# Optimization experiments

Hardware: AMD Instinct MI355X
Metric: run time of the kernel (lower is better)

## Reference

```python
import jax, jax.numpy as jnp
import numpy as np

B, T, CTX, D, L, H, FF, NMODES = 1024, 512, 23, 320, 5, 8, 1280, 48
DH = D // H
EPS = 1e-5


def layernorm(x, w, b):
    m = jnp.mean(x, axis=-1, keepdims=True)
    v = jnp.mean(jnp.square(x - m), axis=-1, keepdims=True)
    return (x - m) * jax.lax.rsqrt(v + EPS) * w + b


def cheb_sum(x, c):
    """sum_n c[:, n] * T_n(x) via the Chebyshev recurrence, fused with the
    reduction (Clenshaw-style accumulation, no (B,T,N+1) intermediate).
    x: (B,T) in [-1,1], c: (B, N+1)."""
    t_prev = jnp.ones_like(x)           # T_0
    t_cur = x                           # T_1
    acc = c[:, 0:1] * t_prev + c[:, 1:2] * t_cur

    def step(carry, cn):
        tp, tc, a = carry
        tn = 2.0 * x * tc - tp          # T_{n+1}
        return (tc, tn, a + cn[:, None] * tn), None

    (_, _, acc), _ = jax.lax.scan(step, (t_prev, t_cur, acc),
                                  jnp.swapaxes(c[:, 2:], 0, 1))
    return acc


def _forward(k_norm, ctx, W_e, b_e, cls, ln1_w, ln1_b, W_in, b_in, W_out, b_out,
             ln2_w, ln2_b, W1, b1, W2, b2, hln_w, hln_b, Wh1, bh1, Wh2, bh2):
    Bc = ctx.shape[0]
    # elem_proj: Linear(1, D) applied per scalar token -> (B, CTX, D)
    tok = ctx[..., None] * W_e + b_e
    x = jnp.concatenate([jnp.broadcast_to(cls, (Bc, 1, D)), tok], axis=1)  # (B, 24, D)

    def layer(x, p):
        l1w, l1b, win, bin_, wout, bout, l2w, l2b, w1, b1_, w2, b2_ = p
        # --- pre-norm self attention ---
        h = layernorm(x, l1w, l1b)
        qkv = h @ win.T + bin_                      # (B, S, 3D)
        q, k, v = jnp.split(qkv, 3, axis=-1)
        S = x.shape[1]
        q = q.reshape(Bc, S, H, DH)
        k = k.reshape(Bc, S, H, DH)
        v = v.reshape(Bc, S, H, DH)
        scores = jnp.einsum('bqhd,bkhd->bhqk', q, k) / np.sqrt(DH).astype(np.float32)
        a = jax.nn.softmax(scores, axis=-1)
        o = jnp.einsum('bhqk,bkhd->bqhd', a, v).reshape(Bc, S, D)
        x = x + o @ wout.T + bout
        # --- pre-norm FFN ---
        h2 = layernorm(x, l2w, l2b)
        x = x + jax.nn.gelu(h2 @ w1.T + b1_, approximate=False) @ w2.T + b2_
        return x, None

    x, _ = jax.lax.scan(layer, x, (ln1_w, ln1_b, W_in, b_in, W_out, b_out,
                                   ln2_w, ln2_b, W1, b1, W2, b2))
    h = layernorm(x[:, 0], hln_w, hln_b)            # CLS pooling + head LN
    c = jax.nn.gelu(h @ Wh1.T + bh1, approximate=False) @ Wh2.T + bh2  # (B, N+1)
    z = cheb_sum(k_norm, c)
    return jax.nn.sigmoid(z)


def setup_inputs() -> dict:
    key = jax.random.key(0)
    ks = jax.random.split(key, 24)
    rn = lambda k, sh, s=0.02: jax.random.normal(k, sh, jnp.float32) * s
    return {
        'k_norm': jax.random.uniform(ks[0], (B, T), jnp.float32, -1.0, 1.0),
        'ctx': jax.random.normal(ks[1], (B, CTX), jnp.float32),
        'W_e': rn(ks[2], (D,), 0.5),
        'b_e': jnp.zeros((D,), jnp.float32),
        'cls': rn(ks[3], (1, 1, D)),
        'ln1_w': jnp.ones((L, D), jnp.float32),
        'ln1_b': jnp.zeros((L, D), jnp.float32),
        'W_in': rn(ks[4], (L, 3 * D, D)),
        'b_in': jnp.zeros((L, 3 * D), jnp.float32),
        'W_out': rn(ks[5], (L, D, D)),
        'b_out': jnp.zeros((L, D), jnp.float32),
        'ln2_w': jnp.ones((L, D), jnp.float32),
        'ln2_b': jnp.zeros((L, D), jnp.float32),
        'W1': rn(ks[6], (L, FF, D)),
        'b1': jnp.zeros((L, FF), jnp.float32),
        'W2': rn(ks[7], (L, D, FF)),
        'b2': jnp.zeros((L, D), jnp.float32),
        'hln_w': jnp.ones((D,), jnp.float32),
        'hln_b': jnp.zeros((D,), jnp.float32),
        'Wh1': rn(ks[8], (D, D)),
        'bh1': jnp.zeros((D,), jnp.float32),
        'Wh2': rn(ks[9], (NMODES + 1, D)),
        'bh2': jnp.zeros((NMODES + 1,), jnp.float32),
    }


def reference(k_norm, ctx, W_e, b_e, cls, ln1_w, ln1_b, W_in, b_in, W_out, b_out,
              ln2_w, ln2_b, W1, b1, W2, b2, hln_w, hln_b, Wh1, bh1, Wh2, bh2):
    return _forward(k_norm, ctx, W_e, b_e, cls, ln1_w, ln1_b, W_in, b_in, W_out,
                    b_out, ln2_w, ln2_b, W1, b1, W2, b2, hln_w, hln_b, Wh1, bh1,
                    Wh2, bh2)
```

## Files before the change

kernel.cpp:

```cpp
#include <hip/hip_runtime.h>
#include <hip/hip_bf16.h>
#include <math.h>

#define B_SZ 1024
#define T_SZ 512
#define CTX_N 23
#define D 320
#define L_LAYERS 5
#define H 8
#define FF 1280
#define NM1 49
#define S 24
#define DH 40
#define M_ROWS (B_SZ * S)

typedef unsigned short ushort_t;
typedef __attribute__((ext_vector_type(8))) short bfrag8;
typedef __attribute__((ext_vector_type(4))) float facc4;

__device__ __forceinline__ float wave_sum(float v) {
#pragma unroll
  for (int off = 32; off > 0; off >>= 1) v += __shfl_xor(v, off, 64);
  return v;
}

__device__ __forceinline__ float gelu_fast(float x) {
  float t = __builtin_amdgcn_exp2f(x * (2.30211416f + 0.10294404f * x * x));
  return x - x * __builtin_amdgcn_rcpf(t + 1.0f);
}

__device__ __forceinline__ ushort_t f2b(float x) {
  __hip_bfloat16 h = __float2bfloat16(x);
  return *reinterpret_cast<ushort_t*>(&h);
}

__device__ __forceinline__ float b2f(ushort_t u) {
  __hip_bfloat16 h = *reinterpret_cast<__hip_bfloat16*>(&u);
  return __bfloat162float(h);
}

#define GLOAD_LDS16(g, l)                                     \
  __builtin_amdgcn_global_load_lds(                           \
      (const __attribute__((address_space(1))) void*)(g),     \
      (__attribute__((address_space(3))) void*)(l), 16, 0, 0)

__global__ __launch_bounds__(256) void conv_all(
    const float* __restrict__ w_in, const float* __restrict__ w_out,
    const float* __restrict__ w1, const float* __restrict__ w2,
    const float* __restrict__ wh1, ushort_t* __restrict__ dst) {
  int i = blockIdx.x * 256 + threadIdx.x;
  const float* src;
  int off;
  if (i < 384000)       { src = w_in;  off = i; }
  else if (i < 512000)  { src = w_out; off = i - 384000; }
  else if (i < 1024000) { src = w1;    off = i - 512000; }
  else if (i < 1536000) { src = w2;    off = i - 1024000; }
  else                  { src = wh1;   off = i - 1536000; }
  float4 v = ((const float4*)src)[off];
  ushort4 o;
  o.x = f2b(v.x); o.y = f2b(v.y); o.z = f2b(v.z); o.w = f2b(v.w);
  ((ushort4*)dst)[i] = o;
}

__global__ __launch_bounds__(256) void embed_kernel(
    const float* __restrict__ ctx, const float* __restrict__ W_e,
    const float* __restrict__ b_e, const float* __restrict__ cls,
    float* __restrict__ x) {
  int idx = blockIdx.x * 256 + threadIdx.x;
  int d = idx % D;
  int s = (idx / D) % S;
  int b = idx / (D * S);
  float v;
  if (s == 0)
    v = cls[d];
  else
    v = ctx[b * CTX_N + (s - 1)] * W_e[d] + b_e[d];
  x[idx] = v;
}

__global__ __launch_bounds__(256) void ln_kernel(
    const float* __restrict__ X, const float* __restrict__ w,
    const float* __restrict__ b, ushort_t* __restrict__ Y,
    int inStride, int outStride) {
  int wv = threadIdx.x >> 6;
  int lane = threadIdx.x & 63;
  int row = blockIdx.x * 4 + wv;
  const float* xr = X + (size_t)row * inStride;
  float v[5];
#pragma unroll
  for (int i = 0; i < 5; i++) v[i] = xr[lane + 64 * i];
  float s = v[0] + v[1] + v[2] + v[3] + v[4];
  s = wave_sum(s);
  float m = s * (1.0f / (float)D);
  float sq = 0.f;
#pragma unroll
  for (int i = 0; i < 5; i++) { float d0 = v[i] - m; sq += d0 * d0; }
  sq = wave_sum(sq);
  float inv = 1.0f / sqrtf(sq * (1.0f / (float)D) + 1e-5f);
  ushort_t* yr = Y + (size_t)row * outStride;
#pragma unroll
  for (int i = 0; i < 5; i++) {
    int d = lane + 64 * i;
    yr[d] = f2b((v[i] - m) * inv * w[d] + b[d]);
  }
}

template <int EPI, int NT, int MT>
__global__ __launch_bounds__(256, 3) void gemm_mfma(
    const ushort_t* __restrict__ A, const ushort_t* __restrict__ W,
    const float* __restrict__ bias, const float* __restrict__ R,
    float* __restrict__ C, ushort_t* __restrict__ Cb, int M, int N, int K) {
  constexpr int BM_ = MT * 32, BK = 64;
  constexpr int BN = 32 * NT;
  constexpr int AR = BM_ / 32;
  constexpr int WR = BN / 32;
  __shared__ __align__(16) ushort_t As[BM_ * BK];
  __shared__ __align__(16) ushort_t Ws[BN * BK];

  int tid = threadIdx.x;
  int lane = tid & 63;
  int wv = tid >> 6;
  int wvM = wv & 1, wvN = wv >> 1;
  int laneM = lane & 15;
  int kgrp = lane >> 4;
  int sA = laneM & 7;

  int nbx = gridDim.x;
  int lid = blockIdx.x + nbx * blockIdx.y;
  int nchunk = nbx >> 3;
  int mb = (lid & 7) * nchunk + ((lid >> 3) % nchunk);
  int nb = (lid >> 3) / nchunk;
  int m0 = mb * BM_;
  int n0 = nb * BN;

  facc4 acc[MT][NT];
#pragma unroll
  for (int mt = 0; mt < MT; mt++)
#pragma unroll
    for (int nt = 0; nt < NT; nt++) acc[mt][nt] = (facc4){0.f, 0.f, 0.f, 0.f};

  int srow = tid >> 3;
  int jg = (tid & 7) ^ (srow & 7);
  const ushort_t* Ag = A + (size_t)(m0 + srow) * K + jg * 8;
  const ushort_t* Wg = W + (size_t)(n0 + srow) * K + jg * 8;

  for (int k0 = 0; k0 < K; k0 += BK) {
#pragma unroll
    for (int r = 0; r < AR; r++)
      GLOAD_LDS16(Ag + (size_t)r * 32 * K + k0, As + r * 2048 + tid * 8);
#pragma unroll
    for (int r = 0; r < WR; r++)
      GLOAD_LDS16(Wg + (size_t)r * 32 * K + k0, Ws + r * 2048 + tid * 8);
    __syncthreads();
#pragma unroll
    for (int kc = 0; kc < 2; kc++) {
      int jcol = ((kc * 4 + kgrp) ^ sA) * 8;
      bfrag8 af[MT];
#pragma unroll
      for (int mt = 0; mt < MT; mt++) {
        int row = wvM * (MT * 16) + mt * 16 + laneM;
        af[mt] = *(const bfrag8*)&As[row * 64 + jcol];
      }
#pragma unroll
      for (int nt = 0; nt < NT; nt++) {
        int nrow = wvN * (BN / 2) + nt * 16 + laneM;
        bfrag8 bf = *(const bfrag8*)&Ws[nrow * 64 + jcol];
#pragma unroll
        for (int mt = 0; mt < MT; mt++)
          acc[mt][nt] = __builtin_amdgcn_mfma_f32_16x16x32_bf16(
              bf, af[mt], acc[mt][nt], 0, 0, 0);
      }
    }
    __syncthreads();
  }

#pragma unroll
  for (int mt = 0; mt < MT; mt++) {
    int m = m0 + wvM * (MT * 16) + mt * 16 + laneM;
#pragma unroll
    for (int nt = 0; nt < NT; nt++) {
      int n = n0 + wvN * (BN / 2) + nt * 16 + kgrp * 4;
      float4 bv = *(const float4*)(bias + n);
      facc4 a = acc[mt][nt];
      float v0 = a[0] + bv.x, v1 = a[1] + bv.y, v2 = a[2] + bv.z,
            v3 = a[3] + bv.w;
      size_t off = (size_t)m * N + n;
      if constexpr (EPI == 1) {
        ushort4 o;
        o.x = f2b(gelu_fast(v0)); o.y = f2b(gelu_fast(v1));
        o.z = f2b(gelu_fast(v2)); o.w = f2b(gelu_fast(v3));
        *(ushort4*)(Cb + off) = o;
      } else if constexpr (EPI == 2) {
        float4 r = *(const float4*)(R + off);
        float4 o = {v0 + r.x, v1 + r.y, v2 + r.z, v3 + r.w};
        *(float4*)(C + off) = o;
      } else if constexpr (EPI == 3) {
        float4 o = {gelu_fast(v0), gelu_fast(v1), gelu_fast(v2),
                    gelu_fast(v3)};
        *(float4*)(C + off) = o;
      } else {
        ushort4 o;
        o.x = f2b(v0); o.y = f2b(v1); o.z = f2b(v2); o.w = f2b(v3);
        *(ushort4*)(Cb + off) = o;
      }
    }
  }
}

__global__ __launch_bounds__(256) void attn_kernel(
    const ushort_t* __restrict__ qkv, ushort_t* __restrict__ o) {
  int b = blockIdx.x >> 3;
  int h = blockIdx.x & 7;
  __shared__ __align__(16) float q[S][44];
  __shared__ __align__(16) float v[S][44];
  __shared__ __align__(16) float kT[DH][28];
  __shared__ __align__(16) float sc[S][28];
  int tid = threadIdx.x;
  const ushort_t* base = qkv + (size_t)b * S * (3 * D) + h * DH;

  for (int idx = tid; idx < 720; idx += 256) {
    int t = idx / 240;
    int r = idx % 240;
    int s = r / 10, dg = r % 10;
    ushort4 u = *(const ushort4*)(base + (size_t)s * (3 * D) + t * D + dg * 4);
    float4 f = {b2f(u.x), b2f(u.y), b2f(u.z), b2f(u.w)};
    if (t == 0) {
      *(float4*)&q[s][dg * 4] = f;
    } else if (t == 2) {
      *(float4*)&v[s][dg * 4] = f;
    } else {
      kT[dg * 4 + 0][s] = f.x;
      kT[dg * 4 + 1][s] = f.y;
      kT[dg * 4 + 2][s] = f.z;
      kT[dg * 4 + 3][s] = f.w;
    }
  }
  __syncthreads();

  if (tid < 144) {
    int i = tid / 6, jg = tid % 6;
    facc4 acc = {0.f, 0.f, 0.f, 0.f};
#pragma unroll
    for (int d = 0; d < DH; d++) {
      float qv = q[i][d];
      float4 kv = *(const float4*)&kT[d][jg * 4];
      acc[0] += qv * kv.x; acc[1] += qv * kv.y;
      acc[2] += qv * kv.z; acc[3] += qv * kv.w;
    }
    const float sca = 0.15811388300841897f;
    float4 ov = {acc[0] * sca, acc[1] * sca, acc[2] * sca, acc[3] * sca};
    *(float4*)&sc[i][jg * 4] = ov;
  }
  __syncthreads();

  if (tid < S) {
    float mx = -1e30f;
#pragma unroll
    for (int j = 0; j < S; j++) mx = fmaxf(mx, sc[tid][j]);
    float sum = 0.f;
#pragma unroll
    for (int j = 0; j < S; j++) {
      float e = __expf(sc[tid][j] - mx);
      sc[tid][j] = e;
      sum += e;
    }
    float rr = 1.0f / sum;
#pragma unroll
    for (int j = 0; j < S; j++) sc[tid][j] *= rr;
  }
  __syncthreads();

  if (tid < 240) {
    int i = tid / 10, dg = tid % 10;
    facc4 acc = {0.f, 0.f, 0.f, 0.f};
#pragma unroll
    for (int j = 0; j < S; j++) {
      float p = sc[i][j];
      float4 vv = *(const float4*)&v[j][dg * 4];
      acc[0] += p * vv.x; acc[1] += p * vv.y;
      acc[2] += p * vv.z; acc[3] += p * vv.w;
    }
    ushort4 ov;
    ov.x = f2b(acc[0]); ov.y = f2b(acc[1]);
    ov.z = f2b(acc[2]); ov.w = f2b(acc[3]);
    *(ushort4*)(o + (size_t)b * S * D + (size_t)i * D + h * DH + dg * 4) = ov;
  }
}

__global__ __launch_bounds__(256) void head_cheb(
    const float* __restrict__ g, const float* __restrict__ Wh2,
    const float* __restrict__ bh2, const float* __restrict__ k_norm,
    float* __restrict__ out) {
  int b = blockIdx.x;
  __shared__ float gs[D];
  __shared__ float cs[NM1];
  int tid = threadIdx.x;
  for (int i = tid; i < D; i += 256) gs[i] = g[(size_t)b * D + i];
  __syncthreads();
  if (tid < NM1) {
    const float* wr = Wh2 + (size_t)tid * D;
    float s = bh2[tid];
    for (int d = 0; d < D; d++) s += gs[d] * wr[d];
    cs[tid] = s;
  }
  __syncthreads();
  for (int t = tid; t < T_SZ; t += 256) {
    float xv = k_norm[(size_t)b * T_SZ + t];
    float tp = 1.f, tc = xv;
    float acc = cs[0] + cs[1] * xv;
#pragma unroll
    for (int n = 2; n < NM1; n++) {
      float tn = 2.f * xv * tc - tp;
      acc += cs[n] * tn;
      tp = tc;
      tc = tn;
    }
    out[(size_t)b * T_SZ + t] = 1.f / (1.f + expf(-acc));
  }
}

extern "C" void kernel_launch(void* const* d_in, const int* in_sizes, int n_in,
                              void* d_out, int out_size, void* d_ws,
                              size_t ws_size, hipStream_t stream) {
  const float* k_norm = (const float*)d_in[0];
  const float* ctx    = (const float*)d_in[1];
  const float* W_e    = (const float*)d_in[2];
  const float* b_e    = (const float*)d_in[3];
  const float* cls    = (const float*)d_in[4];
  const float* ln1_w  = (const float*)d_in[5];
  const float* ln1_b  = (const float*)d_in[6];
  const float* W_in   = (const float*)d_in[7];
  const float* b_in   = (const float*)d_in[8];
  const float* W_out  = (const float*)d_in[9];
  const float* b_out  = (const float*)d_in[10];
  const float* ln2_w  = (const float*)d_in[11];
  const float* ln2_b  = (const float*)d_in[12];
  const float* W1     = (const float*)d_in[13];
  const float* b1     = (const float*)d_in[14];
  const float* W2     = (const float*)d_in[15];
  const float* b2     = (const float*)d_in[16];
  const float* hln_w  = (const float*)d_in[17];
  const float* hln_b  = (const float*)d_in[18];
  const float* Wh1    = (const float*)d_in[19];
  const float* bh1    = (const float*)d_in[20];
  const float* Wh2    = (const float*)d_in[21];
  const float* bh2    = (const float*)d_in[22];
  float* out = (float*)d_out;

  float* x = (float*)d_ws;
  ushort_t* hbuf = (ushort_t*)(x + (size_t)M_ROWS * D);
  ushort_t* big = hbuf + (size_t)M_ROWS * D;
  ushort_t* wb_in = big + (size_t)M_ROWS * FF;
  ushort_t* wb_out = wb_in + (size_t)L_LAYERS * 3 * D * D;
  ushort_t* wb1 = wb_out + (size_t)L_LAYERS * D * D;
  ushort_t* wb2 = wb1 + (size_t)L_LAYERS * FF * D;
  ushort_t* wbh1 = wb2 + (size_t)L_LAYERS * D * FF;
  ushort_t* hcls = wbh1 + (size_t)D * D;
  float* ghead = (float*)(hcls + (size_t)B_SZ * D);

  conv_all<<<6100, 256, 0, stream>>>(W_in, W_out, W1, W2, Wh1, wb_in);

  embed_kernel<<<(M_ROWS * D) / 256, 256, 0, stream>>>(ctx, W_e, b_e, cls, x);

  for (int l = 0; l < L_LAYERS; l++) {
    ln_kernel<<<M_ROWS / 4, 256, 0, stream>>>(x, ln1_w + l * D, ln1_b + l * D,
                                              hbuf, D, D);
    gemm_mfma<4, 5, 4><<<dim3(M_ROWS / 128, (3 * D) / 160), 256, 0, stream>>>(
        hbuf, wb_in + (size_t)l * 3 * D * D, b_in + (size_t)l * 3 * D, nullptr,
        nullptr, big, M_ROWS, 3 * D, D);
    attn_kernel<<<B_SZ * H, 256, 0, stream>>>(big, hbuf);
    gemm_mfma<2, 5, 2><<<dim3(M_ROWS / 64, D / 160), 256, 0, stream>>>(
        hbuf, wb_out + (size_t)l * D * D, b_out + (size_t)l * D, x, x, nullptr,
        M_ROWS, D, D);
    ln_kernel<<<M_ROWS / 4, 256, 0, stream>>>(x, ln2_w + l * D, ln2_b + l * D,
                                              hbuf, D, D);
    gemm_mfma<1, 5, 4><<<dim3(M_ROWS / 128, FF / 160), 256, 0, stream>>>(
        hbuf, wb1 + (size_t)l * FF * D, b1 + (size_t)l * FF, nullptr, nullptr,
        big, M_ROWS, FF, D);
    gemm_mfma<2, 5, 2><<<dim3(M_ROWS / 64, D / 160), 256, 0, stream>>>(
        big, wb2 + (size_t)l * D * FF, b2 + (size_t)l * D, x, x, nullptr,
        M_ROWS, D, FF);
  }

  ln_kernel<<<B_SZ / 4, 256, 0, stream>>>(x, hln_w, hln_b, hcls, S * D, D);
  gemm_mfma<3, 5, 2><<<dim3(B_SZ / 64, D / 160), 256, 0, stream>>>(
      hcls, wbh1, bh1, nullptr, ghead, nullptr, B_SZ, D, D);
  head_cheb<<<B_SZ, 256, 0, stream>>>(ghead, Wh2, bh2, k_norm, out);
}
```

Baseline: 1.005 ms.

## Fuse LayerNorm into residual GEMM epilogues and embedding kernel

Result: no change. 994.5 us (-1.1%).

```diff
diff --git a/kernel.cpp b/kernel.cpp
--- a/kernel.cpp
+++ b/kernel.cpp
@@ -62,20 +62,40 @@
   ((ushort4*)dst)[i] = o;
 }
 
-__global__ __launch_bounds__(256) void embed_kernel(
+__global__ __launch_bounds__(256) void embed_ln(
     const float* __restrict__ ctx, const float* __restrict__ W_e,
     const float* __restrict__ b_e, const float* __restrict__ cls,
-    float* __restrict__ x) {
-  int idx = blockIdx.x * 256 + threadIdx.x;
-  int d = idx % D;
-  int s = (idx / D) % S;
-  int b = idx / (D * S);
-  float v;
-  if (s == 0)
-    v = cls[d];
-  else
-    v = ctx[b * CTX_N + (s - 1)] * W_e[d] + b_e[d];
-  x[idx] = v;
+    const float* __restrict__ lnw, const float* __restrict__ lnb,
+    float* __restrict__ x, ushort_t* __restrict__ y) {
+  int wv = threadIdx.x >> 6;
+  int lane = threadIdx.x & 63;
+  int row = blockIdx.x * 4 + wv;
+  int s = row % S;
+  int b = row / S;
+  float cv = (s == 0) ? 0.f : ctx[b * CTX_N + (s - 1)];
+  float v[5];
+#pragma unroll
+  for (int i = 0; i < 5; i++) {
+    int d = lane + 64 * i;
+    v[i] = (s == 0) ? cls[d] : cv * W_e[d] + b_e[d];
+  }
+  float* xr = x + (size_t)row * D;
+#pragma unroll
+  for (int i = 0; i < 5; i++) xr[lane + 64 * i] = v[i];
+  float sm = v[0] + v[1] + v[2] + v[3] + v[4];
+  sm = wave_sum(sm);
+  float m = sm * (1.0f / (float)D);
+  float sq = 0.f;
+#pragma unroll
+  for (int i = 0; i < 5; i++) { float d0 = v[i] - m; sq += d0 * d0; }
+  sq = wave_sum(sq);
+  float inv = 1.0f / sqrtf(sq * (1.0f / (float)D) + 1e-5f);
+  ushort_t* yr = y + (size_t)row * D;
+#pragma unroll
+  for (int i = 0; i < 5; i++) {
+    int d = lane + 64 * i;
+    yr[d] = f2b((v[i] - m) * inv * lnw[d] + lnb[d]);
+  }
 }
 
 __global__ __launch_bounds__(256) void ln_kernel(
@@ -109,13 +129,17 @@
 __global__ __launch_bounds__(256, 3) void gemm_mfma(
     const ushort_t* __restrict__ A, const ushort_t* __restrict__ W,
     const float* __restrict__ bias, const float* __restrict__ R,
-    float* __restrict__ C, ushort_t* __restrict__ Cb, int M, int N, int K) {
+    float* __restrict__ C, ushort_t* __restrict__ Cb,
+    const float* __restrict__ lnw, const float* __restrict__ lnb,
+    int M, int N, int K) {
   constexpr int BM_ = MT * 32, BK = 64;
   constexpr int BN = 32 * NT;
   constexpr int AR = BM_ / 32;
   constexpr int WR = BN / 32;
   __shared__ __align__(16) ushort_t As[BM_ * BK];
   __shared__ __align__(16) ushort_t Ws[BN * BK];
+  __shared__ float psum[2][BM_];
+  __shared__ float psq[2][BM_];
 
   int tid = threadIdx.x;
   int lane = tid & 63;
@@ -174,34 +198,98 @@
     __syncthreads();
   }
 
-#pragma unroll
-  for (int mt = 0; mt < MT; mt++) {
-    int m = m0 + wvM * (MT * 16) + mt * 16 + laneM;
-#pragma unroll
-    for (int nt = 0; nt < NT; nt++) {
-      int n = n0 + wvN * (BN / 2) + nt * 16 + kgrp * 4;
-      float4 bv = *(const float4*)(bias + n);
-      facc4 a = acc[mt][nt];
-      float v0 = a[0] + bv.x, v1 = a[1] + bv.y, v2 = a[2] + bv.z,
-            v3 = a[3] + bv.w;
-      size_t off = (size_t)m * N + n;
-      if constexpr (EPI == 1) {
+  if constexpr (EPI == 5) {
+    float rs[MT], rq[MT];
+#pragma unroll
+    for (int mt = 0; mt < MT; mt++) { rs[mt] = 0.f; rq[mt] = 0.f; }
+#pragma unroll
+    for (int mt = 0; mt < MT; mt++) {
+      int m = m0 + wvM * (MT * 16) + mt * 16 + laneM;
+#pragma unroll
+      for (int nt = 0; nt < NT; nt++) {
+        int n = n0 + wvN * (BN / 2) + nt * 16 + kgrp * 4;
+        float4 bv = *(const float4*)(bias + n);
+        size_t off = (size_t)m * N + n;
+        float4 r = *(const float4*)(R + off);
+        facc4 a = acc[mt][nt];
+        a[0] += bv.x + r.x; a[1] += bv.y + r.y;
+        a[2] += bv.z + r.z; a[3] += bv.w + r.w;
+        acc[mt][nt] = a;
+        rs[mt] += a[0] + a[1] + a[2] + a[3];
+        rq[mt] += a[0] * a[0] + a[1] * a[1] + a[2] * a[2] + a[3] * a[3];
+      }
+    }
+#pragma unroll
+    for (int mt = 0; mt < MT; mt++) {
+      rs[mt] += __shfl_xor(rs[mt], 16, 64);
+      rs[mt] += __shfl_xor(rs[mt], 32, 64);
+      rq[mt] += __shfl_xor(rq[mt], 16, 64);
+      rq[mt] += __shfl_xor(rq[mt], 32, 64);
+    }
+    if (lane < 16) {
+#pragma unroll
+      for (int mt = 0; mt < MT; mt++) {
+        int lr = wvM * (MT * 16) + mt * 16 + laneM;
+        psum[wvN][lr] = rs[mt];
+        psq[wvN][lr] = rq[mt];
+      }
+    }
+    __syncthreads();
+#pragma unroll
+    for (int mt = 0; mt < MT; mt++) {
+      int lr = wvM * (MT * 16) + mt * 16 + laneM;
+      int m = m0 + lr;
+      float ts = psum[0][lr] + psum[1][lr];
+      float tq = psq[0][lr] + psq[1][lr];
+      float mean = ts * (1.0f / (float)D);
+      float var = tq * (1.0f / (float)D) - mean * mean;
+      float inv = 1.0f / sqrtf(var + 1e-5f);
+#pragma unroll
+      for (int nt = 0; nt < NT; nt++) {
+        int n = n0 + wvN * (BN / 2) + nt * 16 + kgrp * 4;
+        size_t off = (size_t)m * N + n;
+        facc4 a = acc[mt][nt];
+        *(float4*)(C + off) = (float4){a[0], a[1], a[2], a[3]};
+        float4 w4 = *(const float4*)(lnw + n);
+        float4 b4 = *(const float4*)(lnb + n);
         ushort4 o;
-        o.x = f2b(gelu_fast(v0)); o.y = f2b(gelu_fast(v1));
-        o.z = f2b(gelu_fast(v2)); o.w = f2b(gelu_fast(v3));
+        o.x = f2b((a[0] - mean) * inv * w4.x + b4.x);
+        o.y = f2b((a[1] - mean) * inv * w4.y + b4.y);
+        o.z = f2b((a[2] - mean) * inv * w4.z + b4.z);
+        o.w = f2b((a[3] - mean) * inv * w4.w + b4.w);
         *(ushort4*)(Cb + off) = o;
-      } else if constexpr (EPI == 2) {
-        float4 r = *(const float4*)(R + off);
-        float4 o = {v0 + r.x, v1 + r.y, v2 + r.z, v3 + r.w};
-        *(float4*)(C + off) = o;
-      } else if constexpr (EPI == 3) {
-        float4 o = {gelu_fast(v0), gelu_fast(v1), gelu_fast(v2),
-                    gelu_fast(v3)};
-        *(float4*)(C + off) = o;
-      } else {
-        ushort4 o;
-        o.x = f2b(v0); o.y = f2b(v1); o.z = f2b(v2); o.w = f2b(v3);
-        *(ushort4*)(Cb + off) = o;
+      }
+    }
+  } else {
+#pragma unroll
+    for (int mt = 0; mt < MT; mt++) {
+      int m = m0 + wvM * (MT * 16) + mt * 16 + laneM;
+#pragma unroll
+      for (int nt = 0; nt < NT; nt++) {
+        int n = n0 + wvN * (BN / 2) + nt * 16 + kgrp * 4;
+        float4 bv = *(const float4*)(bias + n);
+        facc4 a = acc[mt][nt];
+        float v0 = a[0] + bv.x, v1 = a[1] + bv.y, v2 = a[2] + bv.z,
+              v3 = a[3] + bv.w;
+        size_t off = (size_t)m * N + n;
+        if constexpr (EPI == 1) {
+          ushort4 o;
+          o.x = f2b(gelu_fast(v0)); o.y = f2b(gelu_fast(v1));
+          o.z = f2b(gelu_fast(v2)); o.w = f2b(gelu_fast(v3));
+          *(ushort4*)(Cb + off) = o;
+        } else if constexpr (EPI == 2) {
+          float4 r = *(const float4*)(R + off);
+          float4 o = {v0 + r.x, v1 + r.y, v2 + r.z, v3 + r.w};
+          *(float4*)(C + off) = o;
+        } else if constexpr (EPI == 3) {
+          float4 o = {gelu_fast(v0), gelu_fast(v1), gelu_fast(v2),
+                      gelu_fast(v3)};
+          *(float4*)(C + off) = o;
+        } else {
+          ushort4 o;
+          o.x = f2b(v0); o.y = f2b(v1); o.z = f2b(v2); o.w = f2b(v3);
+          *(ushort4*)(Cb + off) = o;
+        }
       }
     }
   }
@@ -357,33 +445,38 @@
   ushort_t* wbh1 = wb2 + (size_t)L_LAYERS * D * FF;
   ushort_t* hcls = wbh1 + (size_t)D * D;
   float* ghead = (float*)(hcls + (size_t)B_SZ * D);
+  ushort_t* abuf = big + (size_t)M_ROWS * 960;
 
   conv_all<<<6100, 256, 0, stream>>>(W_in, W_out, W1, W2, Wh1, wb_in);
 
-  embed_kernel<<<(M_ROWS * D) / 256, 256, 0, stream>>>(ctx, W_e, b_e, cls, x);
+  embed_ln<<<M_ROWS / 4, 256, 0, stream>>>(ctx, W_e, b_e, cls, ln1_w, ln1_b,
+                                           x, hbuf);
 
   for (int l = 0; l < L_LAYERS; l++) {
-    ln_kernel<<<M_ROWS / 4, 256, 0, stream>>>(x, ln1_w + l * D, ln1_b + l * D,
-                                              hbuf, D, D);
     gemm_mfma<4, 5, 4><<<dim3(M_ROWS / 128, (3 * D) / 160), 256, 0, stream>>>(
         hbuf, wb_in + (size_t)l * 3 * D * D, b_in + (size_t)l * 3 * D, nullptr,
-        nullptr, big, M_ROWS, 3 * D, D);
-    attn_kernel<<<B_SZ * H, 256, 0, stream>>>(big, hbuf);
-    gemm_mfma<2, 5, 2><<<dim3(M_ROWS / 64, D / 160), 256, 0, stream>>>(
-        hbuf, wb_out + (size_t)l * D * D, b_out + (size_t)l * D, x, x, nullptr,
-        M_ROWS, D, D);
-    ln_kernel<<<M_ROWS / 4, 256, 0, stream>>>(x, ln2_w + l * D, ln2_b + l * D,
-                                              hbuf, D, D);
+        nullptr, big, nullptr, nullptr, M_ROWS, 3 * D, D);
+    attn_kernel<<<B_SZ * H, 256, 0, stream>>>(big, abuf);
+    gemm_mfma<5, 10, 2><<<dim3(M_ROWS / 64, 1), 256, 0, stream>>>(
+        abuf, wb_out + (size_t)l * D * D, b_out + (size_t)l * D, x, x, hbuf,
+        ln2_w + (size_t)l * D, ln2_b + (size_t)l * D, M_ROWS, D, D);
     gemm_mfma<1, 5, 4><<<dim3(M_ROWS / 128, FF / 160), 256, 0, stream>>>(
         hbuf, wb1 + (size_t)l * FF * D, b1 + (size_t)l * FF, nullptr, nullptr,
-        big, M_ROWS, FF, D);
-    gemm_mfma<2, 5, 2><<<dim3(M_ROWS / 64, D / 160), 256, 0, stream>>>(
-        big, wb2 + (size_t)l * D * FF, b2 + (size_t)l * D, x, x, nullptr,
-        M_ROWS, D, FF);
+        big, nullptr, nullptr, M_ROWS, FF, D);
+    if (l + 1 < L_LAYERS) {
+      gemm_mfma<5, 10, 2><<<dim3(M_ROWS / 64, 1), 256, 0, stream>>>(
+          big, wb2 + (size_t)l * D * FF, b2 + (size_t)l * D, x, x, hbuf,
+          ln1_w + (size_t)(l + 1) * D, ln1_b + (size_t)(l + 1) * D,
+          M_ROWS, D, FF);
+    } else {
+      gemm_mfma<2, 5, 2><<<dim3(M_ROWS / 64, D / 160), 256, 0, stream>>>(
+          big, wb2 + (size_t)l * D * FF, b2 + (size_t)l * D, x, x, nullptr,
+          nullptr, nullptr, M_ROWS, D, FF);
+    }
   }
 
   ln_kernel<<<B_SZ / 4, 256, 0, stream>>>(x, hln_w, hln_b, hcls, S * D, D);
   gemm_mfma<3, 5, 2><<<dim3(B_SZ / 64, D / 160), 256, 0, stream>>>(
-      hcls, wbh1, bh1, nullptr, ghead, nullptr, B_SZ, D, D);
+      hcls, wbh1, bh1, nullptr, ghead, nullptr, nullptr, nullptr, B_SZ, D, D);
   head_cheb<<<B_SZ, 256, 0, stream>>>(ghead, Wh2, bh2, k_norm, out);
 }
```
